# Performance work log

Hardware: AMD Instinct MI355X
Metric: run time of the kernel (lower is better)

Reference implementation:

```python
import jax, jax.numpy as jnp
import numpy as np

GRID_SIZE = 5
SPLINE_ORDER = 3
NUM_EXPERTS = 8
TOP_K = 2
CAP_FACTOR = 1.25
TEMP = 1.0
GDHW = (4, 4, 4)


def make_grid(in_features):
    # efficient-KAN grid buffer: grid_range=[-1,1], extended by spline_order on each side
    h = 2.0 / GRID_SIZE
    g = jnp.arange(-SPLINE_ORDER, GRID_SIZE + SPLINE_ORDER + 1, dtype=jnp.float32) * h - 1.0
    return jnp.broadcast_to(g, (in_features, g.shape[0]))


def b_splines(x, grid):
    # x: (N, in) -> (N, in, GRID_SIZE + SPLINE_ORDER) Cox-de Boor bases
    x = x[:, :, None]
    bases = ((x >= grid[:, :-1]) & (x < grid[:, 1:])).astype(x.dtype)
    for k in range(1, SPLINE_ORDER + 1):
        left = (x - grid[:, : -(k + 1)]) / (grid[:, k:-1] - grid[:, : -(k + 1)])
        right = (grid[:, k + 1:] - x) / (grid[:, k + 1:] - grid[:, 1:-k])
        bases = left * bases[:, :, :-1] + right * bases[:, :, 1:]
    return bases


def kan_linear(x, base_w, spline_w, scaler, grid):
    base = jax.nn.silu(x) @ base_w.T
    bs = b_splines(x, grid)                                   # (N, in, coef)
    spline = jnp.einsum('nic,oic->no', bs, spline_w * scaler[:, :, None])
    return base + spline


def layernorm(x, w, b, eps=1e-5):
    mu = x.mean(-1, keepdims=True)
    var = x.var(-1, keepdims=True)
    return (x - mu) / jnp.sqrt(var + eps) * w + b


def setup_inputs() -> dict:
    key = jax.random.key(0)
    ks = jax.random.split(key, 12)
    Cf, hidden, E, nc = 256, 170, NUM_EXPERTS, 2
    coef = GRID_SIZE + SPLINE_ORDER
    def nrm(k, shape, scale):
        return jax.random.normal(k, shape, dtype=jnp.float32) * scale
    return {
        'fpn_feat': nrm(ks[0], (8, 254, 32, 32, 32), 1.0),
        'seg_logits': nrm(ks[1], (8, 2, 32, 32, 32), 1.0),
        'ln_r_w': jnp.ones((Cf,), jnp.float32),
        'ln_r_b': jnp.zeros((Cf,), jnp.float32),
        'ln_h_w': jnp.ones((Cf,), jnp.float32),
        'ln_h_b': jnp.zeros((Cf,), jnp.float32),
        'router_w': nrm(ks[2], (E, Cf), Cf ** -0.5),
        'router_b': jnp.zeros((E,), jnp.float32),
        'bw1': nrm(ks[3], (E, hidden, Cf), Cf ** -0.5),
        'sw1': nrm(ks[4], (E, hidden, Cf, coef), 0.1 * Cf ** -0.5),
        'sc1': nrm(ks[5], (E, hidden, Cf), Cf ** -0.5),
        'bw2': nrm(ks[6], (E, Cf, hidden), hidden ** -0.5),
        'sw2': nrm(ks[7], (E, Cf, hidden, coef), 0.1 * hidden ** -0.5),
        'sc2': nrm(ks[8], (E, Cf, hidden), hidden ** -0.5),
        'cls_bw': nrm(ks[9], (nc, Cf), Cf ** -0.5),
        'cls_sw': nrm(ks[10], (nc, Cf, coef), 0.1 * Cf ** -0.5),
        'cls_sc': nrm(ks[11], (nc, Cf), Cf ** -0.5),
        'grid_cf': make_grid(Cf),
        'grid_hid': make_grid(hidden),
    }


def reference(fpn_feat, seg_logits, ln_r_w, ln_r_b, ln_h_w, ln_h_b,
              router_w, router_b, bw1, sw1, sc1, bw2, sw2, sc2,
              cls_bw, cls_sw, cls_sc, grid_cf, grid_hid):
    fused = jnp.concatenate([fpn_feat, seg_logits], axis=1)   # (B, Cf, D, H, W)
    B, C, D, H, W = fused.shape
    gd, gh, gw = GDHW
    dp, hp, wp = D // gd, H // gh, W // gw
    # split into gd*gh*gw blocks per sample
    blk = fused.reshape(B, C, gd, dp, gh, hp, gw, wp)
    blk = blk.transpose(0, 2, 4, 6, 1, 3, 5, 7).reshape(-1, C, dp, hp, wp)
    vec = blk.mean(axis=(2, 3, 4))                            # (N, Cf) global avg pool

    N = vec.shape[0]
    E = NUM_EXPERTS
    x_norm = layernorm(vec, ln_r_w, ln_r_b)
    scores = (x_norm @ router_w.T + router_b) / TEMP          # (N, E)
    top_val, top_idx = jax.lax.top_k(scores, TOP_K)
    top_w = jax.nn.softmax(top_val, axis=-1)
    capacity = int(CAP_FACTOR * N * TOP_K / E) + 1

    onehot = top_idx[None] == jnp.arange(E)[:, None, None]    # (E, N, K)
    sel = onehot.any(-1)                                      # (E, N)
    pos = jnp.cumsum(sel.astype(jnp.int32), axis=1)           # rank among selected (1-based)
    keep = sel & (pos <= capacity)                            # capacity drop = first-come order
    w = (top_w[None] * onehot.astype(top_w.dtype)).sum(-1)    # (E, N) combine weights

    def expert(bw1e, sw1e, sc1e, bw2e, sw2e, sc2e):
        h = kan_linear(x_norm, bw1e, sw1e, sc1e, grid_cf)
        h = jax.nn.gelu(h, approximate=False)                 # torch nn.GELU default (erf)
        return kan_linear(h, bw2e, sw2e, sc2e, grid_hid)

    y_all = jax.vmap(expert)(bw1, sw1, sc1, bw2, sw2, sc2)    # (E, N, Cf)
    out = jnp.einsum('en,enc->nc', keep.astype(vec.dtype) * w, y_all)

    conf = scores.max(-1)                                     # (N,)
    logits_blk = kan_linear(layernorm(out, ln_h_w, ln_h_b), cls_bw, cls_sw, cls_sc, grid_cf)
    P = gd * gh * gw
    weight = jax.nn.softmax(conf.reshape(B, P), axis=-1)[:, :, None]
    logits = (logits_blk.reshape(B, P, -1) * weight).sum(1)   # (B, num_classes)
    return logits
```

## Files before the change

### kernel.cpp

```cpp
#include <hip/hip_runtime.h>
#include <math.h>

#define CF 256
#define HID 170
#define NE 8
#define NTOK 512
#define K1 2304
#define K2P 1536
#define CAPACITY 161

typedef __bf16 bf16x8 __attribute__((ext_vector_type(8)));
typedef unsigned short u16x8 __attribute__((ext_vector_type(8)));
typedef float f32x4 __attribute__((ext_vector_type(4)));

__device__ __forceinline__ float silu_f(float x) { return x / (1.0f + expf(-x)); }
__device__ __forceinline__ float gelu_f(float x) {
    return 0.5f * x * (1.0f + erff(x * 0.70710678118654752f));
}

__device__ __forceinline__ unsigned short f2bf(float f) {
    unsigned int u = __float_as_uint(f);
    u = u + 0x7fffu + ((u >> 16) & 1u);
    return (unsigned short)(u >> 16);
}

__device__ __forceinline__ void bspline8(float x, float bs[8]) {
    float b[11];
#pragma unroll
    for (int j = 0; j < 11; ++j) {
        float g0 = (float)(j - 3) * 0.4f - 1.0f;
        float g1 = (float)(j - 2) * 0.4f - 1.0f;
        b[j] = (x >= g0 && x < g1) ? 1.0f : 0.0f;
    }
#pragma unroll
    for (int k = 1; k <= 3; ++k) {
        float inv = 2.5f / (float)k;
#pragma unroll
        for (int j = 0; j < 10 - (k - 1); ++j) {
            float gj   = (float)(j - 3) * 0.4f - 1.0f;
            float gjk1 = (float)(j - 2 + k) * 0.4f - 1.0f;
            b[j] = (x - gj) * inv * b[j] + (gjk1 - x) * inv * b[j + 1];
        }
    }
#pragma unroll
    for (int c = 0; c < 8; ++c) bs[c] = b[c];
}

__global__ __launch_bounds__(256) void mega_front_kernel(const float* __restrict__ fpn,
                                                         const float* __restrict__ seg,
                                                         const float* __restrict__ bw1,
                                                         const float* __restrict__ sw1,
                                                         const float* __restrict__ sc1,
                                                         const float* __restrict__ bw2,
                                                         const float* __restrict__ sw2,
                                                         const float* __restrict__ sc2,
                                                         float* __restrict__ vec,
                                                         unsigned short* __restrict__ W1,
                                                         unsigned short* __restrict__ W2,
                                                         float* __restrict__ out) {
    int id = blockIdx.x, tid = threadIdx.x;
    if (id == 8192 && tid < 16) out[tid] = 0.0f;
    if (id < 8192) {
        int c = id & 255, bd = (id >> 8) & 3, b = id >> 10;
        const float* src = (c < 254) ? fpn + (size_t)(b * 254 + c) * 32768
                                     : seg + (size_t)(b * 2 + (c - 254)) * 32768;
        const float4* s4 = (const float4*)src + (size_t)bd * 8 * 256;
        float s = 0.0f;
#pragma unroll
        for (int it = 0; it < 8; ++it) {
            float4 v = s4[it * 256 + tid];
            s += v.x + v.y + v.z + v.w;
        }
        __shared__ float acc[16];
        if (tid < 16) acc[tid] = 0.0f;
        __syncthreads();
        int bh = tid >> 6, bw = (tid & 7) >> 1;
        atomicAdd(&acc[bh * 4 + bw], s);
        __syncthreads();
        if (tid < 16)
            vec[(size_t)(b * 64 + bd * 16 + tid) * CF + c] = acc[tid] * (1.0f / 512.0f);
    } else if (id < 8192 + NE * HID) {
        int r = id - 8192;
        int o = r % HID, e = r / HID, i = tid;
        size_t oi = (size_t)(e * HID + o) * CF + i;
        unsigned short* row = W1 + (size_t)(e * HID + o) * K1;
        row[i] = f2bf(bw1[oi]);
        float sc = sc1[oi];
        const float* sw = sw1 + oi * 8;
        u16x8 pk;
#pragma unroll
        for (int c = 0; c < 8; ++c) pk[c] = f2bf(sw[c] * sc);
        *(u16x8*)(row + CF + i * 8) = pk;
    } else {
        int r = id - (8192 + NE * HID);
        int o = r & 255, e = r >> 8, t = tid;
        unsigned short* row = W2 + (size_t)(e * CF + o) * K2P;
        if (t < HID) {
            size_t oi = (size_t)(e * CF + o) * HID + t;
            row[t] = f2bf(bw2[oi]);
            float sc = sc2[oi];
            const float* sw = sw2 + oi * 8;
            u16x8 pk;
#pragma unroll
            for (int c = 0; c < 8; ++c) pk[c] = f2bf(sw[c] * sc);
            *(u16x8*)(row + HID + t * 8) = pk;
        } else if (t < HID + 6) {
            row[HID * 9 + (t - HID)] = 0;
        }
    }
}

__global__ __launch_bounds__(256) void ln_score_a1_kernel(const float* __restrict__ vec,
                                                          const float* __restrict__ lnw,
                                                          const float* __restrict__ lnb,
                                                          const float* __restrict__ rw,
                                                          const float* __restrict__ rb,
                                                          float* __restrict__ scores,
                                                          unsigned short* __restrict__ A1,
                                                          unsigned short* __restrict__ A2) {
    int n = blockIdx.x, i = threadIdx.x;
    if (i < 48) {
        int e = i / 6, j = i - e * 6;
        A2[((size_t)e * NTOK + n) * K2P + HID * 9 + j] = 0;
    }
    float v = vec[(size_t)n * CF + i];
    float s1 = v, s2 = v * v;
#pragma unroll
    for (int off = 32; off > 0; off >>= 1) {
        s1 += __shfl_xor(s1, off);
        s2 += __shfl_xor(s2, off);
    }
    __shared__ float rs1[4], rs2[4];
    int lane = i & 63, wid = i >> 6;
    if (lane == 0) { rs1[wid] = s1; rs2[wid] = s2; }
    __syncthreads();
    float tot1 = rs1[0] + rs1[1] + rs1[2] + rs1[3];
    float tot2 = rs2[0] + rs2[1] + rs2[2] + rs2[3];
    float mu = tot1 * (1.0f / CF);
    float var = tot2 * (1.0f / CF) - mu * mu;
    float rsd = rsqrtf(var + 1e-5f);
    float xv = (v - mu) * rsd * lnw[i] + lnb[i];
    unsigned short* r = A1 + (size_t)n * K1;
    r[i] = f2bf(silu_f(xv));
    float bs[8]; bspline8(xv, bs);
    u16x8 pk;
#pragma unroll
    for (int c = 0; c < 8; ++c) pk[c] = f2bf(bs[c]);
    *(u16x8*)(r + CF + i * 8) = pk;
    float p[NE];
#pragma unroll
    for (int e = 0; e < NE; ++e) p[e] = xv * rw[e * CF + i];
#pragma unroll
    for (int off = 32; off > 0; off >>= 1)
#pragma unroll
        for (int e = 0; e < NE; ++e) p[e] += __shfl_xor(p[e], off);
    __shared__ float pacc[4][NE];
    if (lane == 0)
#pragma unroll
        for (int e = 0; e < NE; ++e) pacc[wid][e] = p[e];
    __syncthreads();
    if (i < NE)
        scores[n * NE + i] = pacc[0][i] + pacc[1][i] + pacc[2][i] + pacc[3][i] + rb[i];
}

template <int MODE>
__global__ __launch_bounds__(256) void gemm_mfma_kernel(
        const unsigned short* __restrict__ Ag, const unsigned short* __restrict__ Bg,
        float* __restrict__ C, unsigned short* __restrict__ A2,
        const float* __restrict__ scores, float* __restrict__ cw, float* __restrict__ conf,
        int N, int K, long sA, long sB, long sC, int ldc) {
    __shared__ alignas(16) unsigned char smem[65536];
    int tid = threadIdx.x;
    int lane = tid & 63, w = tid >> 6;

    if (MODE == 1 && blockIdx.x == 3) {
        if (blockIdx.y != 0 || blockIdx.z != 0) return;
        int* ti0 = (int*)smem;
        int* ti1 = ti0 + NTOK;
        float* tw0 = (float*)(ti1 + NTOK);
        float* tw1 = tw0 + NTOK;
#pragma unroll
        for (int half = 0; half < 2; ++half) {
            int t = half * 256 + tid;
            float m1 = -1e30f, m2 = -1e30f; int i1 = 0, i2 = 0;
#pragma unroll
            for (int e = 0; e < NE; ++e) {
                float sc = scores[t * NE + e];
                if (sc > m1) { m2 = m1; i2 = i1; m1 = sc; i1 = e; }
                else if (sc > m2) { m2 = sc; i2 = e; }
            }
            conf[t] = m1;
            float ew = expf(m2 - m1);
            ti0[t] = i1; ti1[t] = i2;
            tw0[t] = 1.0f / (1.0f + ew); tw1[t] = ew / (1.0f + ew);
        }
        __syncthreads();
#pragma unroll
        for (int e2 = 0; e2 < 2; ++e2) {
            int e = w * 2 + e2;
            int cnt = 0;
#pragma unroll
            for (int c = 0; c < NTOK / 64; ++c) {
                int t = c * 64 + lane;
                int h0 = (ti0[t] == e), h1 = (ti1[t] == e);
                int sel = h0 | h1;
                unsigned long long mask = __ballot(sel);
                int pos = cnt + (int)__popcll(mask & ((1ull << lane) - 1ull));
                float wv = 0.f;
                if (sel && pos < CAPACITY) wv = h0 ? tw0[t] : tw1[t];
                cw[e * NTOK + t] = wv;
                cnt += (int)__popcll(mask);
            }
        }
        return;
    }

    unsigned char* AsB = smem;
    unsigned char* BsB = smem + 32768;

    int e = blockIdx.z;
    const unsigned short* A = Ag + (size_t)e * sA;
    const unsigned short* B = Bg + (size_t)e * sB;
    int m0 = blockIdx.y * 64, n0 = blockIdx.x * 64;
    int wr = w >> 1, wc = w & 1;
    int fr = lane & 15, fg = lane >> 4;

    int r0 = tid >> 5, ch = tid & 31;
    int d0 = r0 * 512 + ((ch * 16) ^ ((r0 & 7) << 4));
    const unsigned short* aP = A + (size_t)(m0 + r0) * K + ch * 8;
    const unsigned short* bP = B + (size_t)(n0 + r0) * K + ch * 8;
    bool bOk[8];
#pragma unroll
    for (int q = 0; q < 8; ++q) bOk[q] = (n0 + r0 + q * 8) < N;
    const u16x8 zero8 = {0, 0, 0, 0, 0, 0, 0, 0};

    f32x4 acc[2][2];
#pragma unroll
    for (int i = 0; i < 2; ++i)
#pragma unroll
        for (int j = 0; j < 2; ++j)
#pragma unroll
            for (int r = 0; r < 4; ++r) acc[i][j][r] = 0.f;

    const int steps = K >> 8;
    u16x8 ra[8], rb[8];
#pragma unroll
    for (int q = 0; q < 8; ++q) {
        ra[q] = *(const u16x8*)(aP + (size_t)q * 8 * K);
        rb[q] = bOk[q] ? *(const u16x8*)(bP + (size_t)q * 8 * K) : zero8;
    }

    for (int s = 0; s < steps; ++s) {
        __syncthreads();
#pragma unroll
        for (int q = 0; q < 8; ++q) {
            *(u16x8*)(AsB + d0 + q * 4096) = ra[q];
            *(u16x8*)(BsB + d0 + q * 4096) = rb[q];
        }
        __syncthreads();
        if (s + 1 < steps) {
            int k0 = (s + 1) << 8;
#pragma unroll
            for (int q = 0; q < 8; ++q) {
                ra[q] = *(const u16x8*)(aP + (size_t)q * 8 * K + k0);
                rb[q] = bOk[q] ? *(const u16x8*)(bP + (size_t)q * 8 * K + k0) : zero8;
            }
        }
#pragma unroll
        for (int ks = 0; ks < 8; ++ks) {
            int kb = ks * 64 + fg * 16;
            u16x8 af[2], bf[2];
#pragma unroll
            for (int mf = 0; mf < 2; ++mf) {
                int row = wr * 32 + mf * 16 + fr;
                af[mf] = *(const u16x8*)(AsB + row * 512 + (kb ^ ((row & 7) << 4)));
            }
#pragma unroll
            for (int nf = 0; nf < 2; ++nf) {
                int row = wc * 32 + nf * 16 + fr;
                bf[nf] = *(const u16x8*)(BsB + row * 512 + (kb ^ ((row & 7) << 4)));
            }
#pragma unroll
            for (int mf = 0; mf < 2; ++mf)
#pragma unroll
                for (int nf = 0; nf < 2; ++nf)
                    acc[mf][nf] = __builtin_amdgcn_mfma_f32_16x16x32_bf16(
                        __builtin_bit_cast(bf16x8, af[mf]),
                        __builtin_bit_cast(bf16x8, bf[nf]), acc[mf][nf], 0, 0, 0);
        }
    }

    if (MODE == 1) {
#pragma unroll
        for (int mf = 0; mf < 2; ++mf)
#pragma unroll
            for (int nf = 0; nf < 2; ++nf)
#pragma unroll
                for (int r = 0; r < 4; ++r) {
                    int row = m0 + wr * 32 + mf * 16 + fg * 4 + r;
                    int col = n0 + wc * 32 + nf * 16 + fr;
                    if (col < N) {
                        float g = gelu_f(acc[mf][nf][r]);
                        unsigned short* rr = A2 + ((size_t)e * NTOK + row) * K2P;
                        rr[col] = f2bf(silu_f(g));
                        float bs[8]; bspline8(g, bs);
                        u16x8 pk;
#pragma unroll
                        for (int c = 0; c < 8; ++c) pk[c] = f2bf(bs[c]);
                        *(u16x8*)(rr + HID + col * 8) = pk;
                    }
                }
    } else {
        float* Ce = C + (size_t)e * sC;
#pragma unroll
        for (int mf = 0; mf < 2; ++mf)
#pragma unroll
            for (int nf = 0; nf < 2; ++nf)
#pragma unroll
                for (int r = 0; r < 4; ++r) {
                    int row = m0 + wr * 32 + mf * 16 + fg * 4 + r;
                    int col = n0 + wc * 32 + nf * 16 + fr;
                    if (col < N) Ce[(size_t)row * ldc + col] = acc[mf][nf][r];
                }
    }
}

__global__ __launch_bounds__(256) void combcls_kernel(const float* __restrict__ y,
                                                      const float* __restrict__ cw,
                                                      const float* __restrict__ conf,
                                                      const float* __restrict__ lnw,
                                                      const float* __restrict__ lnb,
                                                      const float* __restrict__ cbw,
                                                      const float* __restrict__ csw,
                                                      const float* __restrict__ csc,
                                                      float* __restrict__ out) {
    int n = blockIdx.x, i = threadIdx.x;
    float v = 0.f;
#pragma unroll
    for (int e = 0; e < NE; ++e)
        v += cw[e * NTOK + n] * y[((size_t)(e * NTOK + n)) * CF + i];
    float s1 = v, s2 = v * v;
#pragma unroll
    for (int off = 32; off > 0; off >>= 1) {
        s1 += __shfl_xor(s1, off);
        s2 += __shfl_xor(s2, off);
    }
    __shared__ float rA[4], rB[4], rP0[4], rP1[4];
    int lane = i & 63, wid = i >> 6;
    if (lane == 0) { rA[wid] = s1; rB[wid] = s2; }
    __syncthreads();
    float tot1 = rA[0] + rA[1] + rA[2] + rA[3];
    float tot2 = rB[0] + rB[1] + rB[2] + rB[3];
    float mu = tot1 * (1.0f / CF);
    float var = tot2 * (1.0f / CF) - mu * mu;
    float rs = rsqrtf(var + 1e-5f);
    float xh = (v - mu) * rs * lnw[i] + lnb[i];
    float si = silu_f(xh);
    float bs[8]; bspline8(xh, bs);
    float p0 = si * cbw[i], p1 = si * cbw[CF + i];
    float sp0 = 0.f, sp1 = 0.f;
#pragma unroll
    for (int c = 0; c < 8; ++c) {
        sp0 += bs[c] * csw[(size_t)i * 8 + c];
        sp1 += bs[c] * csw[(size_t)(CF + i) * 8 + c];
    }
    p0 += sp0 * csc[i];
    p1 += sp1 * csc[CF + i];
#pragma unroll
    for (int off = 32; off > 0; off >>= 1) {
        p0 += __shfl_xor(p0, off);
        p1 += __shfl_xor(p1, off);
    }
    if (lane == 0) { rP0[wid] = p0; rP1[wid] = p1; }
    __syncthreads();
    if (i < 64) {
        int b = n >> 6;
        float cf = conf[b * 64 + i];
        float mx = cf;
#pragma unroll
        for (int off = 32; off > 0; off >>= 1) mx = fmaxf(mx, __shfl_xor(mx, off));
        float ev = expf(cf - mx);
        float sum = ev;
#pragma unroll
        for (int off = 32; off > 0; off >>= 1) sum += __shfl_xor(sum, off);
        if (i == 0) {
            float wself = expf(conf[n] - mx) / sum;
            float l0 = rP0[0] + rP0[1] + rP0[2] + rP0[3];
            float l1 = rP1[0] + rP1[1] + rP1[2] + rP1[3];
            atomicAdd(&out[b * 2 + 0], wself * l0);
            atomicAdd(&out[b * 2 + 1], wself * l1);
        }
    }
}

extern "C" void kernel_launch(void* const* d_in, const int* in_sizes, int n_in,
                              void* d_out, int out_size, void* d_ws, size_t ws_size,
                              hipStream_t stream) {
    const float* fpn      = (const float*)d_in[0];
    const float* seg      = (const float*)d_in[1];
    const float* ln_r_w   = (const float*)d_in[2];
    const float* ln_r_b   = (const float*)d_in[3];
    const float* ln_h_w   = (const float*)d_in[4];
    const float* ln_h_b   = (const float*)d_in[5];
    const float* router_w = (const float*)d_in[6];
    const float* router_b = (const float*)d_in[7];
    const float* bw1      = (const float*)d_in[8];
    const float* sw1      = (const float*)d_in[9];
    const float* sc1      = (const float*)d_in[10];
    const float* bw2      = (const float*)d_in[11];
    const float* sw2      = (const float*)d_in[12];
    const float* sc2      = (const float*)d_in[13];
    const float* cls_bw   = (const float*)d_in[14];
    const float* cls_sw   = (const float*)d_in[15];
    const float* cls_sc   = (const float*)d_in[16];
    float* out = (float*)d_out;

    float* ws = (float*)d_ws;
    float* vec    = ws;
    float* scores = vec + 131072;
    float* cw     = scores + 4096;
    float* conf   = cw + 4096;
    float* yall   = conf + 512;
    unsigned short* A1b = (unsigned short*)(yall + 1048576);
    unsigned short* W1b = A1b + (size_t)NTOK * K1;
    unsigned short* A2b = W1b + (size_t)NE * HID * K1;
    unsigned short* W2b = A2b + (size_t)NE * NTOK * K2P;

    mega_front_kernel<<<dim3(8192 + NE * HID + 2048), dim3(256), 0, stream>>>(
        fpn, seg, bw1, sw1, sc1, bw2, sw2, sc2, vec, W1b, W2b, out);
    ln_score_a1_kernel<<<dim3(NTOK), dim3(256), 0, stream>>>(vec, ln_r_w, ln_r_b, router_w,
                                                             router_b, scores, A1b, A2b);
    gemm_mfma_kernel<1><<<dim3(4, 8, NE), dim3(256), 0, stream>>>(
        A1b, W1b, nullptr, A2b, scores, cw, conf, HID, K1, 0L, (long)HID * K1, 0L, 0);
    gemm_mfma_kernel<0><<<dim3(4, 8, NE), dim3(256), 0, stream>>>(
        A2b, W2b, yall, nullptr, nullptr, nullptr, nullptr, CF, K2P, (long)NTOK * K2P,
        (long)CF * K2P, (long)NTOK * CF, CF);
    combcls_kernel<<<dim3(NTOK), dim3(256), 0, stream>>>(yall, cw, conf, ln_h_w, ln_h_b,
                                                         cls_bw, cls_sw, cls_sc, out);
}
```

Before: 114.4 us.

## Split-K both expert GEMMs and move the GELU/B-spline epilogue into a reduce kernel

```diff
diff --git a/kernel.cpp b/kernel.cpp
--- a/kernel.cpp
+++ b/kernel.cpp
@@ -8,6 +8,8 @@
 #define K1 2304
 #define K2P 1536
 #define CAPACITY 161
+#define SPLIT1 3
+#define SPLIT2 2
 
 typedef __bf16 bf16x8 __attribute__((ext_vector_type(8)));
 typedef unsigned short u16x8 __attribute__((ext_vector_type(8)));
@@ -163,12 +165,12 @@
         scores[n * NE + i] = pacc[0][i] + pacc[1][i] + pacc[2][i] + pacc[3][i] + rb[i];
 }
 
-template <int MODE>
+template <int MODE, int SPLIT>
 __global__ __launch_bounds__(256) void gemm_mfma_kernel(
         const unsigned short* __restrict__ Ag, const unsigned short* __restrict__ Bg,
-        float* __restrict__ C, unsigned short* __restrict__ A2,
+        float* __restrict__ Ppart,
         const float* __restrict__ scores, float* __restrict__ cw, float* __restrict__ conf,
-        int N, int K, long sA, long sB, long sC, int ldc) {
+        int N, int K, int ksl, long sA, long sB, int ldc) {
     __shared__ alignas(16) unsigned char smem[65536];
     int tid = threadIdx.x;
     int lane = tid & 63, w = tid >> 6;
@@ -218,9 +220,10 @@
     unsigned char* AsB = smem;
     unsigned char* BsB = smem + 32768;
 
-    int e = blockIdx.z;
-    const unsigned short* A = Ag + (size_t)e * sA;
-    const unsigned short* B = Bg + (size_t)e * sB;
+    int z = blockIdx.z, e = z / SPLIT, sp = z % SPLIT;
+    int koff = sp * ksl;
+    const unsigned short* A = Ag + (size_t)e * sA + koff;
+    const unsigned short* B = Bg + (size_t)e * sB + koff;
     int m0 = blockIdx.y * 64, n0 = blockIdx.x * 64;
     int wr = w >> 1, wc = w & 1;
     int fr = lane & 15, fg = lane >> 4;
@@ -242,7 +245,7 @@
 #pragma unroll
             for (int r = 0; r < 4; ++r) acc[i][j][r] = 0.f;
 
-    const int steps = K >> 8;
+    const int steps = ksl >> 8;
     u16x8 ra[8], rb[8];
 #pragma unroll
     for (int q = 0; q < 8; ++q) {
@@ -290,39 +293,34 @@
         }
     }
 
-    if (MODE == 1) {
-#pragma unroll
-        for (int mf = 0; mf < 2; ++mf)
-#pragma unroll
-            for (int nf = 0; nf < 2; ++nf)
-#pragma unroll
-                for (int r = 0; r < 4; ++r) {
-                    int row = m0 + wr * 32 + mf * 16 + fg * 4 + r;
-                    int col = n0 + wc * 32 + nf * 16 + fr;
-                    if (col < N) {
-                        float g = gelu_f(acc[mf][nf][r]);
-                        unsigned short* rr = A2 + ((size_t)e * NTOK + row) * K2P;
-                        rr[col] = f2bf(silu_f(g));
-                        float bs[8]; bspline8(g, bs);
-                        u16x8 pk;
-#pragma unroll
-                        for (int c = 0; c < 8; ++c) pk[c] = f2bf(bs[c]);
-                        *(u16x8*)(rr + HID + col * 8) = pk;
-                    }
-                }
-    } else {
-        float* Ce = C + (size_t)e * sC;
-#pragma unroll
-        for (int mf = 0; mf < 2; ++mf)
-#pragma unroll
-            for (int nf = 0; nf < 2; ++nf)
-#pragma unroll
-                for (int r = 0; r < 4; ++r) {
-                    int row = m0 + wr * 32 + mf * 16 + fg * 4 + r;
-                    int col = n0 + wc * 32 + nf * 16 + fr;
-                    if (col < N) Ce[(size_t)row * ldc + col] = acc[mf][nf][r];
-                }
-    }
+    float* P = Ppart + (size_t)z * NTOK * ldc;
+#pragma unroll
+    for (int mf = 0; mf < 2; ++mf)
+#pragma unroll
+        for (int nf = 0; nf < 2; ++nf)
+#pragma unroll
+            for (int r = 0; r < 4; ++r) {
+                int row = m0 + wr * 32 + mf * 16 + fg * 4 + r;
+                int col = n0 + wc * 32 + nf * 16 + fr;
+                if (col < N) P[(size_t)row * ldc + col] = acc[mf][nf][r];
+            }
+}
+
+__global__ __launch_bounds__(192) void reduce1_kernel(const float* __restrict__ Hpart,
+                                                      unsigned short* __restrict__ A2) {
+    int n = blockIdx.x, e = blockIdx.y, t = threadIdx.x;
+    if (t >= HID) return;
+    size_t idx = ((size_t)(e * SPLIT1) * NTOK + n) * HID + t;
+    const size_t S = (size_t)NTOK * HID;
+    float h = Hpart[idx] + Hpart[idx + S] + Hpart[idx + 2 * S];
+    float g = gelu_f(h);
+    unsigned short* rr = A2 + ((size_t)e * NTOK + n) * K2P;
+    rr[t] = f2bf(silu_f(g));
+    float bs[8]; bspline8(g, bs);
+    u16x8 pk;
+#pragma unroll
+    for (int c = 0; c < 8; ++c) pk[c] = f2bf(bs[c]);
+    *(u16x8*)(rr + HID + t * 8) = pk;
 }
 
 __global__ __launch_bounds__(256) void combcls_kernel(const float* __restrict__ y,
@@ -337,8 +335,11 @@
     int n = blockIdx.x, i = threadIdx.x;
     float v = 0.f;
 #pragma unroll
-    for (int e = 0; e < NE; ++e)
-        v += cw[e * NTOK + n] * y[((size_t)(e * NTOK + n)) * CF + i];
+    for (int e = 0; e < NE; ++e) {
+        size_t i0 = ((size_t)(e * SPLIT2) * NTOK + n) * CF + i;
+        const size_t S = (size_t)NTOK * CF;
+        v += cw[e * NTOK + n] * (y[i0] + y[i0 + S]);
+    }
     float s1 = v, s2 = v * v;
 #pragma unroll
     for (int off = 32; off > 0; off >>= 1) {
@@ -420,8 +421,9 @@
     float* scores = vec + 131072;
     float* cw     = scores + 4096;
     float* conf   = cw + 4096;
-    float* yall   = conf + 512;
-    unsigned short* A1b = (unsigned short*)(yall + 1048576);
+    float* Hpart  = conf + 512;
+    float* Ypart  = Hpart + (size_t)SPLIT1 * NE * NTOK * HID;
+    unsigned short* A1b = (unsigned short*)(Ypart + (size_t)SPLIT2 * NE * NTOK * CF);
     unsigned short* W1b = A1b + (size_t)NTOK * K1;
     unsigned short* A2b = W1b + (size_t)NE * HID * K1;
     unsigned short* W2b = A2b + (size_t)NE * NTOK * K2P;
@@ -430,11 +432,12 @@
         fpn, seg, bw1, sw1, sc1, bw2, sw2, sc2, vec, W1b, W2b, out);
     ln_score_a1_kernel<<<dim3(NTOK), dim3(256), 0, stream>>>(vec, ln_r_w, ln_r_b, router_w,
                                                              router_b, scores, A1b, A2b);
-    gemm_mfma_kernel<1><<<dim3(4, 8, NE), dim3(256), 0, stream>>>(
-        A1b, W1b, nullptr, A2b, scores, cw, conf, HID, K1, 0L, (long)HID * K1, 0L, 0);
-    gemm_mfma_kernel<0><<<dim3(4, 8, NE), dim3(256), 0, stream>>>(
-        A2b, W2b, yall, nullptr, nullptr, nullptr, nullptr, CF, K2P, (long)NTOK * K2P,
-        (long)CF * K2P, (long)NTOK * CF, CF);
-    combcls_kernel<<<dim3(NTOK), dim3(256), 0, stream>>>(yall, cw, conf, ln_h_w, ln_h_b,
+    gemm_mfma_kernel<1, SPLIT1><<<dim3(4, 8, NE * SPLIT1), dim3(256), 0, stream>>>(
+        A1b, W1b, Hpart, scores, cw, conf, HID, K1, K1 / SPLIT1, 0L, (long)HID * K1, HID);
+    reduce1_kernel<<<dim3(NTOK, NE), dim3(192), 0, stream>>>(Hpart, A2b);
+    gemm_mfma_kernel<0, SPLIT2><<<dim3(4, 8, NE * SPLIT2), dim3(256), 0, stream>>>(
+        A2b, W2b, Ypart, nullptr, nullptr, nullptr, CF, K2P, K2P / SPLIT2,
+        (long)NTOK * K2P, (long)CF * K2P, CF);
+    combcls_kernel<<<dim3(NTOK), dim3(256), 0, stream>>>(Ypart, cw, conf, ln_h_w, ln_h_b,
                                                          cls_bw, cls_sw, cls_sc, out);
 }
```

New measurement: 114.7 us. No clear change (+0.3%).
